# Kernel optimization log

Measured on AMD Instinct MI355X. Metric: run time of the kernel, lower is better.

## Reference

```python
import jax, jax.numpy as jnp
import numpy as np

N_NODES = 100000
N_EDGES = 1600000
N_GRAPHS = 128


def _gcn_norm(edge_index, n_nodes):
    # Add self-loops, then symmetric normalization deg^-1/2 * A_hat * deg^-1/2 (PyG GCNConv default).
    loops = jnp.arange(n_nodes, dtype=edge_index.dtype)
    src = jnp.concatenate([edge_index[0], loops])
    dst = jnp.concatenate([edge_index[1], loops])
    deg = jax.ops.segment_sum(jnp.ones_like(src, dtype=jnp.float32), dst, num_segments=n_nodes)
    dinv = jnp.where(deg > 0, jax.lax.rsqrt(deg), 0.0)
    norm = dinv[src] * dinv[dst]  # [E + N]
    return src, dst, norm


def _gcn_conv(x, W, b, src, dst, norm, n_nodes):
    h = x @ W                      # [N, out] linear transform first (small GEMM)
    msg = h[src] * norm[:, None]   # gather + per-edge scale
    out = jax.ops.segment_sum(msg, dst, num_segments=n_nodes)  # scatter-add
    return out + b


def setup_inputs() -> dict:
    key = jax.random.key(0)
    ks = jax.random.split(key, 6)
    x = jax.random.normal(ks[0], (N_NODES, 3), dtype=jnp.float32)
    edge_index = jax.random.randint(ks[1], (2, N_EDGES), 0, N_NODES, dtype=jnp.int64)
    batch = jnp.sort(jax.random.randint(ks[2], (N_NODES,), 0, N_GRAPHS, dtype=jnp.int64))
    W1 = jax.random.normal(ks[3], (3, 64), dtype=jnp.float32) * (1.0 / np.sqrt(3.0))
    b1 = jnp.zeros((64,), dtype=jnp.float32)
    W2 = jax.random.normal(ks[4], (64, 128), dtype=jnp.float32) * (1.0 / np.sqrt(64.0))
    b2 = jnp.zeros((128,), dtype=jnp.float32)
    return {"x": x, "edge_index": edge_index, "batch": batch,
            "W1": W1, "b1": b1, "W2": W2, "b2": b2}


def reference(x, edge_index, batch, W1, b1, W2, b2):
    n_nodes = x.shape[0]
    src, dst, norm = _gcn_norm(edge_index, n_nodes)
    h = jax.nn.relu(_gcn_conv(x, W1, b1, src, dst, norm, n_nodes))
    h = _gcn_conv(h, W2, b2, src, dst, norm, n_nodes)
    # global mean pool over graphs in the batch
    sums = jax.ops.segment_sum(h, batch, num_segments=N_GRAPHS)
    counts = jax.ops.segment_sum(jnp.ones((n_nodes,), dtype=h.dtype), batch, num_segments=N_GRAPHS)
    return sums / jnp.maximum(counts, 1.0)[:, None]
```

## Files before the change

kernel.cpp:

```cpp
#include <hip/hip_runtime.h>
#include <hip/hip_bf16.h>


typedef __hip_bfloat16 bf16;
#define NGRAPH 128
#define NSLICE 8
#define TILE_S 4096
#define CAPLG  13
#define SCAP   12288

__device__ __forceinline__ float b2f(bf16 v) { return __bfloat162float(v); }
__device__ __forceinline__ float fld(const void* p, long long i, int isbf) {
    return isbf ? b2f(((const bf16*)p)[i]) : ((const float*)p)[i];
}
__device__ __forceinline__ int ild(const void* p, long long i, int is64) {
    return is64 ? (int)((const long long*)p)[i] : ((const int*)p)[i];
}
__device__ __forceinline__ int probe_is64(const void* ei) {
    int lane = threadIdx.x & 63;
    const int* w = (const int*)ei;
    unsigned long long bz = __ballot(w[2 * lane + 1] == 0);
    return (__popcll(bz) >= 56) ? 1 : 0;
}
__device__ __forceinline__ int probe_isbf(const void* x) {
    int lane = threadIdx.x & 63;
    const unsigned short* u = (const unsigned short*)x;
    int e0 = (u[2 * lane] >> 7) & 0xFF;
    int e1 = (u[2 * (lane + 64)] >> 7) & 0xFF;
    int good = __popcll(__ballot(e0 >= 90 && e0 <= 135))
             + __popcll(__ballot(e1 >= 90 && e1 <= 135));
    return (good >= 96) ? 1 : 0;
}

__global__ void k_split(const void* __restrict__ ei, unsigned* __restrict__ edges2,
                        int* __restrict__ gcur, float4* __restrict__ P4,
                        int E, int NB) {
    for (int k = blockIdx.x * 256 + threadIdx.x; k < NSLICE * NGRAPH * 16;
         k += gridDim.x * 256)
        P4[k] = make_float4(0.f, 0.f, 0.f, 0.f);
    __shared__ int hist[512], scan_[512], gbase[512], lcur[512];
    __shared__ int2 stage[TILE_S];
    int is64 = probe_is64(ei);
    long long base = (long long)blockIdx.x * TILE_S;
    int lim = (int)min((long long)TILE_S, (long long)E - base);
    for (int b = threadIdx.x; b < 512; b += 256) hist[b] = 0;
    __syncthreads();
    int dreg[16], sreg[16];
#pragma unroll
    for (int j = 0; j < 16; ++j) {
        int k = threadIdx.x + (j << 8);
        if (k < lim) {
            int d = ild(ei, (long long)E + base + k, is64);
            int s = ild(ei, base + k, is64);
            dreg[j] = d; sreg[j] = s;
            atomicAdd(&hist[d >> 8], 1);
        } else dreg[j] = -1;
    }
    __syncthreads();
    {
        int i0 = threadIdx.x, i1 = threadIdx.x + 256;
        scan_[i0] = hist[i0]; scan_[i1] = hist[i1];
        __syncthreads();
        for (int d = 1; d < 512; d <<= 1) {
            int t0 = (i0 >= d) ? scan_[i0 - d] : 0;
            int t1 = (i1 >= d) ? scan_[i1 - d] : 0;
            __syncthreads();
            scan_[i0] += t0; scan_[i1] += t1;
            __syncthreads();
        }
        int e0 = scan_[i0] - hist[i0];
        int e1 = scan_[i1] - hist[i1];
        __syncthreads();
        scan_[i0] = e0; scan_[i1] = e1;
        __syncthreads();
    }
    for (int b = threadIdx.x; b < NB; b += 256) {
        lcur[b] = scan_[b];
        gbase[b] = hist[b] ? atomicAdd(&gcur[b], hist[b]) : 0;
    }
    __syncthreads();
#pragma unroll
    for (int j = 0; j < 16; ++j) {
        if (dreg[j] >= 0) {
            int p = atomicAdd(&lcur[dreg[j] >> 8], 1);
            stage[p] = make_int2(dreg[j], sreg[j]);
        }
    }
    __syncthreads();
    for (int t = threadIdx.x; t < lim; t += 256) {
        int2 r = stage[t];
        int b = r.x >> 8;
        edges2[((size_t)b << CAPLG) + gbase[b] + (t - scan_[b])] =
            (unsigned)r.y | ((unsigned)(r.x & 255) << 24);
    }
}

__global__ void k_bscan(const int* __restrict__ gcur, int* __restrict__ bktoff,
                        int N, int NB) {
    __shared__ int sb[512];
    int i = threadIdx.x;
    int nloc = (i < NB) ? min(256, N - (i << 8)) : 0;
    int vb = ((i < NB) ? gcur[i] : 0) + nloc;
    sb[i] = vb;
    __syncthreads();
    for (int d = 1; d < 512; d <<= 1) {
        int tb = (i >= d) ? sb[i - d] : 0;
        __syncthreads();
        sb[i] += tb;
        __syncthreads();
    }
    if (i < NB) bktoff[i] = sb[i] - vb;
    if (i == NB - 1) bktoff[NB] = sb[i];
}

__global__ void k_sort(const unsigned* __restrict__ edges2, const void* __restrict__ batch,
                       const void* __restrict__ x, const void* __restrict__ ei,
                       const int* __restrict__ gcur, const int* __restrict__ bktoff,
                       unsigned* __restrict__ meta, int* __restrict__ row_ptr,
                       float* __restrict__ dinv, float4* __restrict__ xs,
                       int* __restrict__ start, int N, int Etot) {
    __shared__ int hist[256], loff[257], lcur[256], sc[256];
    __shared__ unsigned gdeg[256];
    __shared__ unsigned stage[SCAP];
    int b = blockIdx.x;
    int node0 = b << 8;
    int nloc = min(256, N - node0);
    int is64 = probe_is64(ei);
    int isbf = probe_isbf(x);
    int i = threadIdx.x;
    if (i < nloc) hist[i] = 0;
    __syncthreads();
    size_t rbase = (size_t)b << CAPLG;
    int rcnt = gcur[b];
    for (int t = i; t < rcnt; t += 256) {
        unsigned r = edges2[rbase + t];
        atomicAdd(&hist[r >> 24], 1);
    }
    __syncthreads();
    int v = (i < nloc) ? hist[i] + 1 : 0;
    sc[i] = v;
    __syncthreads();
    for (int d = 1; d < 256; d <<= 1) {
        int t = (i >= d) ? sc[i - d] : 0;
        __syncthreads();
        sc[i] += t;
        __syncthreads();
    }
    if (i < nloc) loff[i] = sc[i] - v;
    if (i == nloc - 1) loff[nloc] = sc[i];
    __syncthreads();
    int mbase = bktoff[b];
    if (i < nloc) {
        int node = node0 + i;
        int dg = hist[i];
        float di = rsqrtf((float)(dg + 1));
        dinv[node] = di;
        row_ptr[node] = mbase + loff[i];
        int g = ild(batch, node, is64);
        int gp = (node == 0) ? -1 : ild(batch, node - 1, is64);
        for (int q = gp + 1; q <= g; ++q) start[q] = node;
        if (node == N - 1)
            for (int q = g + 1; q <= NGRAPH; ++q) start[q] = N;
        xs[node] = make_float4(di * fld(x, 3LL * node, isbf),
                               di * fld(x, 3LL * node + 1, isbf),
                               di * fld(x, 3LL * node + 2, isbf), 0.0f);
        unsigned gd = ((unsigned)g << 17) | ((unsigned)min(dg, 255) << 24);
        gdeg[i] = gd;
        lcur[i] = loff[i] + 1;
        stage[loff[i]] = (unsigned)node | gd;
    }
    __syncthreads();
    for (int t = i; t < rcnt; t += 256) {
        unsigned r = edges2[rbase + t];
        int dl = (int)(r >> 24);
        int p = atomicAdd(&lcur[dl], 1);
        if (p < SCAP) stage[p] = (r & 0x1FFFFu) | gdeg[dl];
    }
    __syncthreads();
    int total = loff[nloc];
    for (int t = i; t < total; t += 256) meta[mbase + t] = stage[t];
    if (b == 0 && i == 0) row_ptr[N] = Etot;
}

__global__ void k_l1(const float4* __restrict__ xs, const float* __restrict__ dinv,
                     const int* __restrict__ row_ptr, const unsigned* __restrict__ meta,
                     const void* __restrict__ W1, const void* __restrict__ b1,
                     const void* __restrict__ x,
                     bf16* __restrict__ hs1, int N) {
    __shared__ float w[256];
    __shared__ float ag[256][4];
    int isbf = probe_isbf(x);
    if (threadIdx.x < 192) w[threadIdx.x] = fld(W1, threadIdx.x, isbf);
    if (threadIdx.x < 64) w[192 + threadIdx.x] = fld(b1, threadIdx.x, isbf);
    int node0 = blockIdx.x << 8;
    int nloc = min(256, N - node0);
    int i = threadIdx.x;
    if (i < nloc) {
        int node = node0 + i;
        float ax = 0.f, ay = 0.f, az = 0.f;
        int p1 = row_ptr[node + 1];
        for (int p = row_ptr[node]; p < p1; ++p) {
            float4 vv = xs[meta[p] & 0x1FFFFu];
            ax += vv.x; ay += vv.y; az += vv.z;
        }
        float di = dinv[node];
        ag[i][0] = di * ax; ag[i][1] = di * ay; ag[i][2] = di * az;
        ag[i][3] = di;
    }
    __syncthreads();
    for (int t = threadIdx.x; t < (nloc << 6); t += 256) {
        int ii = t >> 6, j = t & 63;
        float acc = ag[ii][0] * w[j] + ag[ii][1] * w[64 + j] + ag[ii][2] * w[128 + j]
                  + w[192 + j];
        hs1[(size_t)(node0 + ii) * 64 + j] = __float2bfloat16(ag[ii][3] * fmaxf(acc, 0.0f));
    }
}

__global__ void k_gather2(const uint4* __restrict__ hs1q, const unsigned* __restrict__ meta,
                          float* __restrict__ P, int Etot, int chunk) {
    int wid = (blockIdx.x * blockDim.x + threadIdx.x) >> 6;
    int lane = threadIdx.x & 63;
    int q = lane >> 3;
    int l8 = lane & 7;
    long long base = (long long)wid * chunk;
    if (base >= Etot) return;
    long long end = base + chunk;
    if (end > Etot) end = Etot;
    float acc[8] = {0.f, 0.f, 0.f, 0.f, 0.f, 0.f, 0.f, 0.f};
    int gcur = -1;
#define GFLUSH()                                                                \
    if (gcur >= 0) {                                                            \
        float* dp = P + (size_t)q * (NGRAPH * 64) + (size_t)gcur * 64 + (l8 << 3); \
        _Pragma("unroll")                                                       \
        for (int k = 0; k < 8; ++k) { atomicAdd(dp + k, acc[k]); acc[k] = 0.f; }\
    }
#define STEP(m, v)                                                              \
    {                                                                           \
        int g = (int)((m >> 17) & 0x7Fu);                                       \
        float w = rsqrtf((float)((m >> 24) & 0xFFu) + 1.0f);                    \
        if (g != gcur) { GFLUSH(); gcur = g; }                                  \
        acc[0] += w * __uint_as_float(v.x << 16);                               \
        acc[1] += w * __uint_as_float(v.x & 0xFFFF0000u);                       \
        acc[2] += w * __uint_as_float(v.y << 16);                               \
        acc[3] += w * __uint_as_float(v.y & 0xFFFF0000u);                       \
        acc[4] += w * __uint_as_float(v.z << 16);                               \
        acc[5] += w * __uint_as_float(v.z & 0xFFFF0000u);                       \
        acc[6] += w * __uint_as_float(v.w << 16);                               \
        acc[7] += w * __uint_as_float(v.w & 0xFFFF0000u);                       \
    }
    long long p = base + q;
    for (; p + 24 < end; p += 32) {
        unsigned m0 = meta[p];
        unsigned m1 = meta[p + 8];
        unsigned m2 = meta[p + 16];
        unsigned m3 = meta[p + 24];
        uint4 v0 = hs1q[(size_t)(m0 & 0x1FFFFu) * 8 + l8];
        uint4 v1 = hs1q[(size_t)(m1 & 0x1FFFFu) * 8 + l8];
        uint4 v2 = hs1q[(size_t)(m2 & 0x1FFFFu) * 8 + l8];
        uint4 v3 = hs1q[(size_t)(m3 & 0x1FFFFu) * 8 + l8];
        STEP(m0, v0) STEP(m1, v1) STEP(m2, v2) STEP(m3, v3)
    }
    for (; p < end; p += 8) {
        unsigned m = meta[p];
        uint4 v = hs1q[(size_t)(m & 0x1FFFFu) * 8 + l8];
        STEP(m, v)
    }
    {
        int g0 = __shfl(gcur, 0);
        if (g0 >= 0 && __all(gcur == g0)) {
#pragma unroll
            for (int k = 0; k < 8; ++k) {
                acc[k] += __shfl_xor(acc[k], 8);
                acc[k] += __shfl_xor(acc[k], 16);
                acc[k] += __shfl_xor(acc[k], 32);
            }
            if (q == 0) {
                float* dp = P + (size_t)(wid & (NSLICE - 1)) * (NGRAPH * 64)
                              + (size_t)g0 * 64 + (l8 << 3);
#pragma unroll
                for (int k = 0; k < 8; ++k) atomicAdd(dp + k, acc[k]);
            }
        } else {
            GFLUSH();
        }
    }
#undef STEP
#undef GFLUSH
}

__global__ void k_out(const float* __restrict__ P, const int* __restrict__ start,
                      const void* __restrict__ W2, const void* __restrict__ b2v,
                      const void* __restrict__ x, void* __restrict__ out) {
    __shared__ float pm[64];
    int isbf = probe_isbf(x);
    int g = blockIdx.x, j = threadIdx.x;
    int c = start[g + 1] - start[g];
    if (j < 64) {
        float v = 0.f;
        for (int s = 0; s < NSLICE; ++s) v += P[(size_t)s * NGRAPH * 64 + g * 64 + j];
        pm[j] = (c > 0) ? v / (float)c : 0.0f;
    }
    __syncthreads();
    float acc = 0.0f;
    if (c > 0) {
        acc = fld(b2v, j, isbf);
        for (int k = 0; k < 64; ++k) acc += pm[k] * fld(W2, k * 128 + j, isbf);
    }
    if (isbf) ((bf16*)out)[g * 128 + j] = __float2bfloat16(acc);
    else      ((float*)out)[g * 128 + j] = acc;
}

extern "C" void kernel_launch(void* const* d_in, const int* in_sizes, int n_in,
                              void* d_out, int out_size, void* d_ws, size_t ws_size,
                              hipStream_t stream) {
    const void* x    = d_in[0];
    const void* ei   = d_in[1];
    const void* batch= d_in[2];
    const void* W1   = d_in[3];
    const void* b1   = d_in[4];
    const void* W2   = d_in[5];
    const void* b2   = d_in[6];

    const int N = in_sizes[0] / 3;
    const int E = in_sizes[1] / 2;
    const int Etot = E + N;
    const int NB = (N + 255) / 256;

    char* ws = (char*)d_ws;
    size_t off = 0;
    auto alloc = [&](size_t bytes) {
        size_t o = off;
        off = (off + bytes + 511) & ~(size_t)511;
        return o;
    };
    int* gcur     = (int*)(ws + alloc((size_t)NB * 4));
    int* bktoff   = (int*)(ws + alloc((size_t)(NB + 1) * 4));
    int* start    = (int*)(ws + alloc((size_t)(NGRAPH + 1) * 4));
    int* row_ptr  = (int*)(ws + alloc((size_t)(N + 1) * 4));
    float* dinv   = (float*)(ws + alloc((size_t)N * 4));
    unsigned* edges2 = (unsigned*)(ws + alloc(((size_t)NB << CAPLG) * 4));
    unsigned* meta= (unsigned*)(ws + alloc((size_t)Etot * 4));
    float4* xs    = (float4*)(ws + alloc((size_t)N * 16));
    bf16* hs1     = (bf16*)(ws + alloc((size_t)N * 64 * 2));
    float* P      = (float*)(ws + alloc((size_t)NSLICE * NGRAPH * 64 * 4));
    (void)ws_size;

    (void)hipMemsetAsync(gcur, 0, (size_t)NB * 4, stream);

    const int sb = (E + TILE_S - 1) / TILE_S;

    const int g2blocks = 2048;
    const int g2waves = g2blocks * 4;
    const int chunk = (Etot + g2waves - 1) / g2waves;

    k_split<<<sb, 256, 0, stream>>>(ei, edges2, gcur, (float4*)P, E, NB);
    k_bscan<<<1, 512, 0, stream>>>(gcur, bktoff, N, NB);
    k_sort<<<NB, 256, 0, stream>>>(edges2, batch, x, ei, gcur, bktoff, meta,
                                   row_ptr, dinv, xs, start, N, Etot);
    k_l1<<<NB, 256, 0, stream>>>(xs, dinv, row_ptr, meta, W1, b1, x, hs1, N);
    k_gather2<<<g2blocks, 256, 0, stream>>>((const uint4*)hs1, meta, P, Etot, chunk);
    k_out<<<NGRAPH, 128, 0, stream>>>(P, start, W2, b2, x, d_out);
}
```

Measured before the change: 199.5 us.

## Split degree pass out of sort and fuse layer-1 aggregation into sort kernel

Splits the per-bucket sort into a degree/normalisation kernel and a kernel that fuses the CSR sort with the layer-1 aggregation and transform. The fused kernel reads neighbour indices directly from shared-memory staging, so meta is not re-read from global memory. It also caches up to 4096 bucket entries in registers to avoid a second global read of edges2. In exchange, the degree pass adds an extra read of edges2, the staging capacity shrinks to 8192 entries, and row_ptr/dinv are dropped. Register and LDS pressure may lower occupancy.

After: 182.1 us. 8.7% less time.

```diff
diff --git a/kernel.cpp b/kernel.cpp
--- a/kernel.cpp
+++ b/kernel.cpp
@@ -7,7 +7,7 @@
 #define NSLICE 8
 #define TILE_S 4096
 #define CAPLG  13
-#define SCAP   12288
+#define SCAP   8192
 
 __device__ __forceinline__ float b2f(bf16 v) { return __bfloat162float(v); }
 __device__ __forceinline__ float fld(const void* p, long long i, int isbf) {
@@ -113,15 +113,12 @@
     if (i == NB - 1) bktoff[NB] = sb[i];
 }
 
-__global__ void k_sort(const unsigned* __restrict__ edges2, const void* __restrict__ batch,
-                       const void* __restrict__ x, const void* __restrict__ ei,
-                       const int* __restrict__ gcur, const int* __restrict__ bktoff,
-                       unsigned* __restrict__ meta, int* __restrict__ row_ptr,
-                       float* __restrict__ dinv, float4* __restrict__ xs,
-                       int* __restrict__ start, int N, int Etot) {
-    __shared__ int hist[256], loff[257], lcur[256], sc[256];
-    __shared__ unsigned gdeg[256];
-    __shared__ unsigned stage[SCAP];
+__global__ void k_deg(const unsigned* __restrict__ edges2, const int* __restrict__ gcur,
+                      const void* __restrict__ batch, const void* __restrict__ x,
+                      const void* __restrict__ ei,
+                      float4* __restrict__ xs, int* __restrict__ deg,
+                      int* __restrict__ start, int N) {
+    __shared__ int hist[256];
     int b = blockIdx.x;
     int node0 = b << 8;
     int nloc = min(256, N - node0);
@@ -132,45 +129,84 @@
     __syncthreads();
     size_t rbase = (size_t)b << CAPLG;
     int rcnt = gcur[b];
-    for (int t = i; t < rcnt; t += 256) {
-        unsigned r = edges2[rbase + t];
-        atomicAdd(&hist[r >> 24], 1);
-    }
-    __syncthreads();
-    int v = (i < nloc) ? hist[i] + 1 : 0;
-    sc[i] = v;
-    __syncthreads();
-    for (int d = 1; d < 256; d <<= 1) {
-        int t = (i >= d) ? sc[i - d] : 0;
-        __syncthreads();
-        sc[i] += t;
-        __syncthreads();
-    }
-    if (i < nloc) loff[i] = sc[i] - v;
-    if (i == nloc - 1) loff[nloc] = sc[i];
-    __syncthreads();
-    int mbase = bktoff[b];
+    for (int t = i; t < rcnt; t += 256)
+        atomicAdd(&hist[edges2[rbase + t] >> 24], 1);
+    __syncthreads();
     if (i < nloc) {
         int node = node0 + i;
         int dg = hist[i];
+        deg[node] = dg;
         float di = rsqrtf((float)(dg + 1));
-        dinv[node] = di;
-        row_ptr[node] = mbase + loff[i];
+        xs[node] = make_float4(di * fld(x, 3LL * node, isbf),
+                               di * fld(x, 3LL * node + 1, isbf),
+                               di * fld(x, 3LL * node + 2, isbf), 0.0f);
         int g = ild(batch, node, is64);
         int gp = (node == 0) ? -1 : ild(batch, node - 1, is64);
         for (int q = gp + 1; q <= g; ++q) start[q] = node;
         if (node == N - 1)
             for (int q = g + 1; q <= NGRAPH; ++q) start[q] = N;
-        xs[node] = make_float4(di * fld(x, 3LL * node, isbf),
-                               di * fld(x, 3LL * node + 1, isbf),
-                               di * fld(x, 3LL * node + 2, isbf), 0.0f);
+    }
+}
+
+__global__ void k_sortl1(const unsigned* __restrict__ edges2, const void* __restrict__ batch,
+                         const void* __restrict__ x, const void* __restrict__ ei,
+                         const int* __restrict__ gcur, const int* __restrict__ bktoff,
+                         const int* __restrict__ deg, const float4* __restrict__ xs,
+                         const void* __restrict__ W1, const void* __restrict__ b1,
+                         unsigned* __restrict__ meta, bf16* __restrict__ hs1, int N) {
+    __shared__ int loff[257], lcur[256], sc[256];
+    __shared__ unsigned gdeg[256];
+    __shared__ unsigned stage[SCAP];
+    __shared__ float w[256];
+    __shared__ float ag[256][4];
+    int b = blockIdx.x;
+    int node0 = b << 8;
+    int nloc = min(256, N - node0);
+    int is64 = probe_is64(ei);
+    int isbf = probe_isbf(x);
+    int i = threadIdx.x;
+    if (i < 192) w[i] = fld(W1, i, isbf);
+    if (i < 64) w[192 + i] = fld(b1, i, isbf);
+    size_t rbase = (size_t)b << CAPLG;
+    int rcnt = gcur[b];
+    unsigned rc[16];
+    int ncache = min(rcnt, 4096);
+#pragma unroll
+    for (int j = 0; j < 16; ++j) {
+        int t = i + (j << 8);
+        rc[j] = (t < ncache) ? edges2[rbase + t] : 0xFFFFFFFFu;
+    }
+    int dg = (i < nloc) ? deg[node0 + i] : 0;
+    int v = (i < nloc) ? dg + 1 : 0;
+    sc[i] = v;
+    __syncthreads();
+    for (int d = 1; d < 256; d <<= 1) {
+        int t = (i >= d) ? sc[i - d] : 0;
+        __syncthreads();
+        sc[i] += t;
+        __syncthreads();
+    }
+    if (i < nloc) loff[i] = sc[i] - v;
+    if (i == nloc - 1) loff[nloc] = sc[i];
+    __syncthreads();
+    if (i < nloc) {
+        int node = node0 + i;
+        int g = ild(batch, node, is64);
         unsigned gd = ((unsigned)g << 17) | ((unsigned)min(dg, 255) << 24);
         gdeg[i] = gd;
         lcur[i] = loff[i] + 1;
         stage[loff[i]] = (unsigned)node | gd;
     }
     __syncthreads();
-    for (int t = i; t < rcnt; t += 256) {
+#pragma unroll
+    for (int j = 0; j < 16; ++j) {
+        if (rc[j] != 0xFFFFFFFFu) {
+            int dl = (int)(rc[j] >> 24);
+            int p = atomicAdd(&lcur[dl], 1);
+            if (p < SCAP) stage[p] = (rc[j] & 0x1FFFFu) | gdeg[dl];
+        }
+    }
+    for (int t = 4096 + i; t < rcnt; t += 256) {
         unsigned r = edges2[rbase + t];
         int dl = (int)(r >> 24);
         int p = atomicAdd(&lcur[dl], 1);
@@ -178,37 +214,22 @@
     }
     __syncthreads();
     int total = loff[nloc];
-    for (int t = i; t < total; t += 256) meta[mbase + t] = stage[t];
-    if (b == 0 && i == 0) row_ptr[N] = Etot;
-}
-
-__global__ void k_l1(const float4* __restrict__ xs, const float* __restrict__ dinv,
-                     const int* __restrict__ row_ptr, const unsigned* __restrict__ meta,
-                     const void* __restrict__ W1, const void* __restrict__ b1,
-                     const void* __restrict__ x,
-                     bf16* __restrict__ hs1, int N) {
-    __shared__ float w[256];
-    __shared__ float ag[256][4];
-    int isbf = probe_isbf(x);
-    if (threadIdx.x < 192) w[threadIdx.x] = fld(W1, threadIdx.x, isbf);
-    if (threadIdx.x < 64) w[192 + threadIdx.x] = fld(b1, threadIdx.x, isbf);
-    int node0 = blockIdx.x << 8;
-    int nloc = min(256, N - node0);
-    int i = threadIdx.x;
+    int totc = min(total, SCAP);
+    int mbase = bktoff[b];
+    for (int t = i; t < totc; t += 256) meta[mbase + t] = stage[t];
     if (i < nloc) {
-        int node = node0 + i;
         float ax = 0.f, ay = 0.f, az = 0.f;
-        int p1 = row_ptr[node + 1];
-        for (int p = row_ptr[node]; p < p1; ++p) {
-            float4 vv = xs[meta[p] & 0x1FFFFu];
+        int p1 = min(loff[i + 1], SCAP);
+        for (int p = loff[i]; p < p1; ++p) {
+            float4 vv = xs[stage[p] & 0x1FFFFu];
             ax += vv.x; ay += vv.y; az += vv.z;
         }
-        float di = dinv[node];
+        float di = rsqrtf((float)(dg + 1));
         ag[i][0] = di * ax; ag[i][1] = di * ay; ag[i][2] = di * az;
         ag[i][3] = di;
     }
     __syncthreads();
-    for (int t = threadIdx.x; t < (nloc << 6); t += 256) {
+    for (int t = i; t < (nloc << 6); t += 256) {
         int ii = t >> 6, j = t & 63;
         float acc = ag[ii][0] * w[j] + ag[ii][1] * w[64 + j] + ag[ii][2] * w[128 + j]
                   + w[192 + j];
@@ -336,8 +357,7 @@
     int* gcur     = (int*)(ws + alloc((size_t)NB * 4));
     int* bktoff   = (int*)(ws + alloc((size_t)(NB + 1) * 4));
     int* start    = (int*)(ws + alloc((size_t)(NGRAPH + 1) * 4));
-    int* row_ptr  = (int*)(ws + alloc((size_t)(N + 1) * 4));
-    float* dinv   = (float*)(ws + alloc((size_t)N * 4));
+    int* deg      = (int*)(ws + alloc((size_t)N * 4));
     unsigned* edges2 = (unsigned*)(ws + alloc(((size_t)NB << CAPLG) * 4));
     unsigned* meta= (unsigned*)(ws + alloc((size_t)Etot * 4));
     float4* xs    = (float4*)(ws + alloc((size_t)N * 16));
@@ -355,9 +375,9 @@
 
     k_split<<<sb, 256, 0, stream>>>(ei, edges2, gcur, (float4*)P, E, NB);
     k_bscan<<<1, 512, 0, stream>>>(gcur, bktoff, N, NB);
-    k_sort<<<NB, 256, 0, stream>>>(edges2, batch, x, ei, gcur, bktoff, meta,
-                                   row_ptr, dinv, xs, start, N, Etot);
-    k_l1<<<NB, 256, 0, stream>>>(xs, dinv, row_ptr, meta, W1, b1, x, hs1, N);
+    k_deg<<<NB, 256, 0, stream>>>(edges2, gcur, batch, x, ei, xs, deg, start, N);
+    k_sortl1<<<NB, 256, 0, stream>>>(edges2, batch, x, ei, gcur, bktoff, deg, xs,
+                                     W1, b1, meta, hs1, N);
     k_gather2<<<g2blocks, 256, 0, stream>>>((const uint4*)hs1, meta, P, Etot, chunk);
     k_out<<<NGRAPH, 128, 0, stream>>>(P, start, W2, b2, x, d_out);
 }
```
